# Kernel tuning notes

Hardware: AMD Instinct MI355X
Metric: run time of the kernel (lower is better)

The kernel has to match this reference:

```python
import jax, jax.numpy as jnp
import numpy as np

N, E, IN, H, OUT, G = 50000, 600000, 128, 128, 10, 64


def gcn_conv(x, src, dst, W, b, n):
    # PyG GCNConv: x' = D^{-1/2} (A + I) D^{-1/2} (x W) + b
    h = x @ W
    ones = jnp.ones(src.shape[0], x.dtype)
    deg = jax.ops.segment_sum(ones, dst, num_segments=n) + 1.0  # +1 for self-loop
    dinv = jax.lax.rsqrt(deg)
    norm = dinv[src] * dinv[dst]                                 # [E]
    agg = jax.ops.segment_sum(h[src] * norm[:, None], dst, num_segments=n)
    agg = agg + h * (1.0 / deg)[:, None]                         # self-loop term
    return agg + b


def setup_inputs() -> dict:
    key = jax.random.key(0)
    ks = jax.random.split(key, 12)
    s = 1.0 / np.sqrt(H)
    return {
        "x": jax.random.normal(ks[0], (N, IN), jnp.float32),
        "edge_index": jax.random.randint(ks[1], (2, E), 0, N, dtype=jnp.int32),
        "batch": jnp.sort(jax.random.randint(ks[2], (N,), 0, G, dtype=jnp.int32)),
        "W1": jax.random.normal(ks[3], (IN, H), jnp.float32) * s,
        "b1": jnp.zeros((H,), jnp.float32),
        "W2": jax.random.normal(ks[4], (H, H), jnp.float32) * s,
        "b2": jnp.zeros((H,), jnp.float32),
        "W3": jax.random.normal(ks[5], (H, H), jnp.float32) * s,
        "b3": jnp.zeros((H,), jnp.float32),
        "Wfc": jax.random.normal(ks[6], (H, OUT), jnp.float32) * s,
        "bfc": jnp.zeros((OUT,), jnp.float32),
    }


def reference(x, edge_index, batch, W1, b1, W2, b2, W3, b3, Wfc, bfc):
    src, dst = edge_index[0], edge_index[1]
    h = jax.nn.relu(gcn_conv(x, src, dst, W1, b1, N))
    h = jax.nn.relu(gcn_conv(h, src, dst, W2, b2, N))
    h = jax.nn.relu(gcn_conv(h, src, dst, W3, b3, N))
    # global mean pool over graphs
    sums = jax.ops.segment_sum(h, batch, num_segments=G)
    cnt = jax.ops.segment_sum(jnp.ones(N, h.dtype), batch, num_segments=G)
    pooled = sums / jnp.maximum(cnt, 1.0)[:, None]               # [G, H]
    return pooled @ Wfc + bfc                                    # [G, OUT]
```

## Files before the change

### kernel.cpp

```cpp
#include <hip/hip_runtime.h>


#define N_NODES 50000
#define N_EDGES 600000
#define DIM 128
#define OUT_DIM 10
#define N_GRAPHS 64
#define STRIP 128
#define GR 64

__global__ void zero_kernel(int* __restrict__ p, int n) {
    int i = blockIdx.x * blockDim.x + threadIdx.x;
    for (; i < n; i += gridDim.x * blockDim.x) p[i] = 0;
}

__global__ void hist_kernel(const int* __restrict__ dst, int* __restrict__ deg) {
    int e = blockIdx.x * blockDim.x + threadIdx.x;
    if (e < N_EDGES) atomicAdd(&deg[dst[e]], 1);
}

__global__ void node_prep_kernel(const int* __restrict__ deg, int* __restrict__ start,
                                 float* __restrict__ dinv, float* __restrict__ invdeg,
                                 int* __restrict__ gcur) {
    int i = blockIdx.x * blockDim.x + threadIdx.x;
    if (i < N_NODES) {
        int d = deg[i];
        start[i] = atomicAdd(gcur, d);
        float df = (float)d + 1.0f;
        dinv[i]   = rsqrtf(df);
        invdeg[i] = 1.0f / df;
    }
}

__global__ void csr_build_kernel(const int* __restrict__ src, const int* __restrict__ dst,
                                 const int* __restrict__ start, int* __restrict__ cursor,
                                 const float* __restrict__ dinv,
                                 int2* __restrict__ csr_pair) {
    int e = blockIdx.x * blockDim.x + threadIdx.x;
    if (e < N_EDGES) {
        int s = src[e], d = dst[e];
        int slot = start[d] + atomicAdd(&cursor[d], 1);
        int2 rec;
        rec.x = s;
        rec.y = __float_as_int(dinv[s] * dinv[d]);
        csr_pair[slot] = rec;
    }
}

__global__ __launch_bounds__(256) void gemm_kernel(const float* __restrict__ A,
                                                   const float* __restrict__ W,
                                                   float* __restrict__ C) {
    __shared__ float4 Alds[GR][DIM / 4];
    int row0 = blockIdx.x * GR;
    int tid  = threadIdx.x;
    for (int i = tid; i < GR * (DIM / 4); i += 256) {
        int r = i >> 5, c = i & 31;
        int gr = row0 + r;
        Alds[r][c] = (gr < N_NODES) ? ((const float4*)A)[(size_t)gr * 32 + c]
                                    : make_float4(0.f, 0.f, 0.f, 0.f);
    }
    __syncthreads();
    int tx = tid & 31;
    int ty = tid >> 5;
    float acc[8][4];
#pragma unroll
    for (int r = 0; r < 8; ++r)
#pragma unroll
        for (int c = 0; c < 4; ++c) acc[r][c] = 0.f;
    const float4* W4 = (const float4*)W;
    for (int k = 0; k < DIM; k += 4) {
        float4 a[8];
#pragma unroll
        for (int r = 0; r < 8; ++r) a[r] = Alds[ty * 8 + r][k >> 2];
        float4 w0 = W4[(k + 0) * 32 + tx];
        float4 w1 = W4[(k + 1) * 32 + tx];
        float4 w2 = W4[(k + 2) * 32 + tx];
        float4 w3 = W4[(k + 3) * 32 + tx];
#pragma unroll
        for (int r = 0; r < 8; ++r) {
            acc[r][0] += a[r].x * w0.x + a[r].y * w1.x + a[r].z * w2.x + a[r].w * w3.x;
            acc[r][1] += a[r].x * w0.y + a[r].y * w1.y + a[r].z * w2.y + a[r].w * w3.y;
            acc[r][2] += a[r].x * w0.z + a[r].y * w1.z + a[r].z * w2.z + a[r].w * w3.z;
            acc[r][3] += a[r].x * w0.w + a[r].y * w1.w + a[r].z * w2.w + a[r].w * w3.w;
        }
    }
#pragma unroll
    for (int r = 0; r < 8; ++r) {
        int gr = row0 + ty * 8 + r;
        if (gr < N_NODES) {
            float4 o = make_float4(acc[r][0], acc[r][1], acc[r][2], acc[r][3]);
            ((float4*)C)[(size_t)gr * 32 + tx] = o;
        }
    }
}

__global__ __launch_bounds__(256) void pull_kernel(const float* __restrict__ HW,
                                                   const int2* __restrict__ csr_pair,
                                                   const int* __restrict__ start,
                                                   const int* __restrict__ deg,
                                                   const float* __restrict__ invdeg,
                                                   const float* __restrict__ bias,
                                                   float* __restrict__ Fout) {
    int node = blockIdx.x * 4 + (threadIdx.x >> 6);
    int lane = threadIdx.x & 63;
    if (node >= N_NODES) return;
    const float2* HW2 = (const float2*)HW;
    int st = start[node];
    int dg = deg[node];
    float ax = 0.f, ay = 0.f;
    for (int base = 0; base < dg; base += 64) {
        int m = min(dg - base, 64);
        int2 rec = (lane < m) ? csr_pair[st + base + lane] : make_int2(0, 0);
        int   si = rec.x;
        float wi = __int_as_float(rec.y);
        int idx = 0;
        for (; idx + 8 <= m; idx += 8) {
            int s0 = __shfl(si, idx);     int s1 = __shfl(si, idx + 1);
            int s2 = __shfl(si, idx + 2); int s3 = __shfl(si, idx + 3);
            int s4 = __shfl(si, idx + 4); int s5 = __shfl(si, idx + 5);
            int s6 = __shfl(si, idx + 6); int s7 = __shfl(si, idx + 7);
            float w0 = __shfl(wi, idx);     float w1 = __shfl(wi, idx + 1);
            float w2 = __shfl(wi, idx + 2); float w3 = __shfl(wi, idx + 3);
            float w4 = __shfl(wi, idx + 4); float w5 = __shfl(wi, idx + 5);
            float w6 = __shfl(wi, idx + 6); float w7 = __shfl(wi, idx + 7);
            float2 v0 = HW2[(size_t)s0 * 64 + lane];
            float2 v1 = HW2[(size_t)s1 * 64 + lane];
            float2 v2 = HW2[(size_t)s2 * 64 + lane];
            float2 v3 = HW2[(size_t)s3 * 64 + lane];
            float2 v4 = HW2[(size_t)s4 * 64 + lane];
            float2 v5 = HW2[(size_t)s5 * 64 + lane];
            float2 v6 = HW2[(size_t)s6 * 64 + lane];
            float2 v7 = HW2[(size_t)s7 * 64 + lane];
            ax += v0.x * w0; ay += v0.y * w0;
            ax += v1.x * w1; ay += v1.y * w1;
            ax += v2.x * w2; ay += v2.y * w2;
            ax += v3.x * w3; ay += v3.y * w3;
            ax += v4.x * w4; ay += v4.y * w4;
            ax += v5.x * w5; ay += v5.y * w5;
            ax += v6.x * w6; ay += v6.y * w6;
            ax += v7.x * w7; ay += v7.y * w7;
        }
        for (; idx < m; ++idx) {
            int s = __shfl(si, idx);
            float w = __shfl(wi, idx);
            float2 v = HW2[(size_t)s * 64 + lane];
            ax += v.x * w; ay += v.y * w;
        }
    }
    float iv = invdeg[node];
    float2 hs = HW2[(size_t)node * 64 + lane];
    ax += hs.x * iv; ay += hs.y * iv;
    float2 bb = ((const float2*)bias)[lane];
    ax = fmaxf(ax + bb.x, 0.f);
    ay = fmaxf(ay + bb.y, 0.f);
    float2 o; o.x = ax; o.y = ay;
    ((float2*)Fout)[(size_t)node * 64 + lane] = o;
}

__global__ void bounds_kernel(const int* __restrict__ batch,
                              int* __restrict__ startg, int* __restrict__ endg) {
    int i = blockIdx.x * blockDim.x + threadIdx.x;
    if (i >= N_NODES) return;
    int b = batch[i];
    if (i == 0 || batch[i - 1] != b) startg[b] = i;
    if (i == N_NODES - 1 || batch[i + 1] != b) endg[b] = i + 1;
}

__global__ __launch_bounds__(128) void pool_kernel(const float* __restrict__ F,
                                                   const int* __restrict__ batch,
                                                   float* __restrict__ pooled) {
    int s0 = blockIdx.x * STRIP;
    int f  = threadIdx.x;
    if (s0 >= N_NODES) return;
    int end = min(s0 + STRIP, N_NODES);
    int cur = batch[s0];
    float acc = 0.f;
    for (int n = s0; n < end; ++n) {
        int bn = batch[n];
        if (bn != cur) {
            atomicAdd(&pooled[cur * DIM + f], acc);
            acc = 0.f; cur = bn;
        }
        acc += F[(size_t)n * DIM + f];
    }
    atomicAdd(&pooled[cur * DIM + f], acc);
}

__global__ __launch_bounds__(640) void fc_kernel(const float* __restrict__ pooled,
                                                 const int* __restrict__ startg,
                                                 const int* __restrict__ endg,
                                                 const float* __restrict__ Wfc,
                                                 const float* __restrict__ bfc,
                                                 float* __restrict__ out) {
    int t = threadIdx.x;
    if (t >= N_GRAPHS * OUT_DIM) return;
    int g = t / OUT_DIM, o = t % OUT_DIM;
    int c = endg[g] - startg[g];
    float inv = 1.0f / fmaxf((float)c, 1.0f);
    float acc = bfc[o];
#pragma unroll 8
    for (int k = 0; k < DIM; ++k)
        acc += pooled[g * DIM + k] * inv * Wfc[k * OUT_DIM + o];
    out[g * OUT_DIM + o] = acc;
}

extern "C" void kernel_launch(void* const* d_in, const int* in_sizes, int n_in,
                              void* d_out, int out_size, void* d_ws, size_t ws_size,
                              hipStream_t stream) {
    const float* x    = (const float*)d_in[0];
    const int*   ei   = (const int*)d_in[1];
    const int*   batch= (const int*)d_in[2];
    const float* W1   = (const float*)d_in[3];
    const float* b1   = (const float*)d_in[4];
    const float* W2   = (const float*)d_in[5];
    const float* b2   = (const float*)d_in[6];
    const float* W3   = (const float*)d_in[7];
    const float* b3   = (const float*)d_in[8];
    const float* Wfc  = (const float*)d_in[9];
    const float* bfc  = (const float*)d_in[10];
    float* out = (float*)d_out;

    const int* src = ei;
    const int* dst = ei + N_EDGES;

    char* ws = (char*)d_ws;
    size_t o = 0;
    float* HW   = (float*)(ws + o); o += (size_t)N_NODES * DIM * 4;
    float* PB   = (float*)(ws + o); o += (size_t)N_NODES * DIM * 4;
    int*   deg    = (int*)(ws + o); o += (size_t)N_NODES * 4;
    int*   cursor = (int*)(ws + o); o += (size_t)N_NODES * 4;
    float* pooled = (float*)(ws + o); o += (size_t)N_GRAPHS * DIM * 4;
    int*   startg = (int*)(ws + o); o += (size_t)N_GRAPHS * 4;
    int*   endg   = (int*)(ws + o); o += (size_t)N_GRAPHS * 4;
    int*   gcur   = (int*)(ws + o); o += 4;
    o = (o + 7) & ~(size_t)7;
    int*   startv = (int*)(ws + o); o += (size_t)N_NODES * 4;
    float* dinv   = (float*)(ws + o); o += (size_t)N_NODES * 4;
    float* invdeg = (float*)(ws + o); o += (size_t)N_NODES * 4;
    int2*  csr_pair = (int2*)(ws + o); o += (size_t)N_EDGES * 8;

    const int nzero = 2 * N_NODES + N_GRAPHS * DIM + 2 * N_GRAPHS + 1;

    zero_kernel<<<(nzero + 255) / 256, 256, 0, stream>>>(deg, nzero);
    hist_kernel<<<(N_EDGES + 255) / 256, 256, 0, stream>>>(dst, deg);
    node_prep_kernel<<<(N_NODES + 255) / 256, 256, 0, stream>>>(deg, startv, dinv, invdeg, gcur);
    csr_build_kernel<<<(N_EDGES + 255) / 256, 256, 0, stream>>>(src, dst, startv, cursor,
                                                                dinv, csr_pair);

    const int ggrid = (N_NODES + GR - 1) / GR;
    const int pgrid = (N_NODES + 3) / 4;

    gemm_kernel<<<ggrid, 256, 0, stream>>>(x, W1, HW);
    pull_kernel<<<pgrid, 256, 0, stream>>>(HW, csr_pair, startv, deg, invdeg, b1, PB);
    gemm_kernel<<<ggrid, 256, 0, stream>>>(PB, W2, HW);
    pull_kernel<<<pgrid, 256, 0, stream>>>(HW, csr_pair, startv, deg, invdeg, b2, PB);
    gemm_kernel<<<ggrid, 256, 0, stream>>>(PB, W3, HW);
    pull_kernel<<<pgrid, 256, 0, stream>>>(HW, csr_pair, startv, deg, invdeg, b3, PB);

    bounds_kernel<<<(N_NODES + 255) / 256, 256, 0, stream>>>(batch, startg, endg);
    pool_kernel<<<(N_NODES + STRIP - 1) / STRIP, 128, 0, stream>>>(PB, batch, pooled);
    fc_kernel<<<1, 640, 0, stream>>>(pooled, startg, endg, Wfc, bfc, out);
}
```

Baseline: 441.7 us.

## Replace atomic CSR offsets with prefix scan and split pull across feature halves

Node start offsets were handed out by an atomic counter in arbitrary order. They are now computed by a three-kernel exclusive prefix scan, so each node's edge list sits in node order and consecutive nodes' edges are contiguous. The pull kernel now launches two blocks per group of four nodes, each covering 64 of the 128 features with scalar loads instead of float2. This doubles parallelism and shortens each wave's work, at the cost of re-reading the CSR records and shuffles twice and narrower memory transactions.

```diff
diff --git a/kernel.cpp b/kernel.cpp
--- a/kernel.cpp
+++ b/kernel.cpp
@@ -8,6 +8,7 @@
 #define N_GRAPHS 64
 #define STRIP 128
 #define GR 64
+#define SCAN_G ((N_NODES + 255) / 256)
 
 __global__ void zero_kernel(int* __restrict__ p, int n) {
     int i = blockIdx.x * blockDim.x + threadIdx.x;
@@ -19,17 +20,58 @@
     if (e < N_EDGES) atomicAdd(&deg[dst[e]], 1);
 }
 
-__global__ void node_prep_kernel(const int* __restrict__ deg, int* __restrict__ start,
-                                 float* __restrict__ dinv, float* __restrict__ invdeg,
-                                 int* __restrict__ gcur) {
-    int i = blockIdx.x * blockDim.x + threadIdx.x;
+__global__ __launch_bounds__(256) void scan_local_kernel(const int* __restrict__ deg,
+                                                         int* __restrict__ locx,
+                                                         int* __restrict__ bsum,
+                                                         float* __restrict__ dinv,
+                                                         float* __restrict__ invdeg) {
+    __shared__ int lds[256];
+    int tid = threadIdx.x;
+    int i = blockIdx.x * 256 + tid;
+    int d = (i < N_NODES) ? deg[i] : 0;
+    int v = d;
+    lds[tid] = v;
+    __syncthreads();
+#pragma unroll
+    for (int off = 1; off < 256; off <<= 1) {
+        int t = (tid >= off) ? lds[tid - off] : 0;
+        __syncthreads();
+        v += t;
+        lds[tid] = v;
+        __syncthreads();
+    }
     if (i < N_NODES) {
-        int d = deg[i];
-        start[i] = atomicAdd(gcur, d);
+        locx[i] = v - d;
         float df = (float)d + 1.0f;
         dinv[i]   = rsqrtf(df);
         invdeg[i] = 1.0f / df;
     }
+    if (tid == 255) bsum[blockIdx.x] = v;
+}
+
+__global__ __launch_bounds__(256) void scan_block_kernel(const int* __restrict__ bsum,
+                                                         int* __restrict__ boff) {
+    __shared__ int lds[256];
+    int tid = threadIdx.x;
+    int d = (tid < SCAN_G) ? bsum[tid] : 0;
+    int v = d;
+    lds[tid] = v;
+    __syncthreads();
+#pragma unroll
+    for (int off = 1; off < 256; off <<= 1) {
+        int t = (tid >= off) ? lds[tid - off] : 0;
+        __syncthreads();
+        v += t;
+        lds[tid] = v;
+        __syncthreads();
+    }
+    if (tid < SCAN_G) boff[tid] = v - d;
+}
+
+__global__ void scan_apply_kernel(const int* __restrict__ locx, const int* __restrict__ boff,
+                                  int* __restrict__ startv) {
+    int i = blockIdx.x * blockDim.x + threadIdx.x;
+    if (i < N_NODES) startv[i] = locx[i] + boff[blockIdx.x];
 }
 
 __global__ void csr_build_kernel(const int* __restrict__ src, const int* __restrict__ dst,
@@ -101,13 +143,15 @@
                                                    const float* __restrict__ invdeg,
                                                    const float* __restrict__ bias,
                                                    float* __restrict__ Fout) {
-    int node = blockIdx.x * 4 + (threadIdx.x >> 6);
+    int wid  = threadIdx.x >> 6;
     int lane = threadIdx.x & 63;
+    int half = blockIdx.x & 1;
+    int node = (blockIdx.x >> 1) * 4 + wid;
     if (node >= N_NODES) return;
-    const float2* HW2 = (const float2*)HW;
+    int f = half * 64 + lane;
     int st = start[node];
     int dg = deg[node];
-    float ax = 0.f, ay = 0.f;
+    float ax = 0.f;
     for (int base = 0; base < dg; base += 64) {
         int m = min(dg - base, 64);
         int2 rec = (lane < m) ? csr_pair[st + base + lane] : make_int2(0, 0);
@@ -123,38 +167,26 @@
             float w2 = __shfl(wi, idx + 2); float w3 = __shfl(wi, idx + 3);
             float w4 = __shfl(wi, idx + 4); float w5 = __shfl(wi, idx + 5);
             float w6 = __shfl(wi, idx + 6); float w7 = __shfl(wi, idx + 7);
-            float2 v0 = HW2[(size_t)s0 * 64 + lane];
-            float2 v1 = HW2[(size_t)s1 * 64 + lane];
-            float2 v2 = HW2[(size_t)s2 * 64 + lane];
-            float2 v3 = HW2[(size_t)s3 * 64 + lane];
-            float2 v4 = HW2[(size_t)s4 * 64 + lane];
-            float2 v5 = HW2[(size_t)s5 * 64 + lane];
-            float2 v6 = HW2[(size_t)s6 * 64 + lane];
-            float2 v7 = HW2[(size_t)s7 * 64 + lane];
-            ax += v0.x * w0; ay += v0.y * w0;
-            ax += v1.x * w1; ay += v1.y * w1;
-            ax += v2.x * w2; ay += v2.y * w2;
-            ax += v3.x * w3; ay += v3.y * w3;
-            ax += v4.x * w4; ay += v4.y * w4;
-            ax += v5.x * w5; ay += v5.y * w5;
-            ax += v6.x * w6; ay += v6.y * w6;
-            ax += v7.x * w7; ay += v7.y * w7;
+            float v0 = HW[(size_t)s0 * DIM + f];
+            float v1 = HW[(size_t)s1 * DIM + f];
+            float v2 = HW[(size_t)s2 * DIM + f];
+            float v3 = HW[(size_t)s3 * DIM + f];
+            float v4 = HW[(size_t)s4 * DIM + f];
+            float v5 = HW[(size_t)s5 * DIM + f];
+            float v6 = HW[(size_t)s6 * DIM + f];
+            float v7 = HW[(size_t)s7 * DIM + f];
+            ax += v0 * w0 + v1 * w1 + v2 * w2 + v3 * w3
+                + v4 * w4 + v5 * w5 + v6 * w6 + v7 * w7;
         }
         for (; idx < m; ++idx) {
             int s = __shfl(si, idx);
             float w = __shfl(wi, idx);
-            float2 v = HW2[(size_t)s * 64 + lane];
-            ax += v.x * w; ay += v.y * w;
-        }
-    }
-    float iv = invdeg[node];
-    float2 hs = HW2[(size_t)node * 64 + lane];
-    ax += hs.x * iv; ay += hs.y * iv;
-    float2 bb = ((const float2*)bias)[lane];
-    ax = fmaxf(ax + bb.x, 0.f);
-    ay = fmaxf(ay + bb.y, 0.f);
-    float2 o; o.x = ax; o.y = ay;
-    ((float2*)Fout)[(size_t)node * 64 + lane] = o;
+            ax += HW[(size_t)s * DIM + f] * w;
+        }
+    }
+    ax += HW[(size_t)node * DIM + f] * invdeg[node];
+    ax = fmaxf(ax + bias[f], 0.f);
+    Fout[(size_t)node * DIM + f] = ax;
 }
 
 __global__ void bounds_kernel(const int* __restrict__ batch,
@@ -232,23 +264,27 @@
     float* pooled = (float*)(ws + o); o += (size_t)N_GRAPHS * DIM * 4;
     int*   startg = (int*)(ws + o); o += (size_t)N_GRAPHS * 4;
     int*   endg   = (int*)(ws + o); o += (size_t)N_GRAPHS * 4;
-    int*   gcur   = (int*)(ws + o); o += 4;
-    o = (o + 7) & ~(size_t)7;
     int*   startv = (int*)(ws + o); o += (size_t)N_NODES * 4;
     float* dinv   = (float*)(ws + o); o += (size_t)N_NODES * 4;
     float* invdeg = (float*)(ws + o); o += (size_t)N_NODES * 4;
+    int*   locx   = (int*)(ws + o); o += (size_t)N_NODES * 4;
+    int*   bsum   = (int*)(ws + o); o += (size_t)SCAN_G * 4;
+    int*   boff   = (int*)(ws + o); o += (size_t)SCAN_G * 4;
+    o = (o + 7) & ~(size_t)7;
     int2*  csr_pair = (int2*)(ws + o); o += (size_t)N_EDGES * 8;
 
-    const int nzero = 2 * N_NODES + N_GRAPHS * DIM + 2 * N_GRAPHS + 1;
+    const int nzero = 2 * N_NODES + N_GRAPHS * DIM + 2 * N_GRAPHS;
 
     zero_kernel<<<(nzero + 255) / 256, 256, 0, stream>>>(deg, nzero);
     hist_kernel<<<(N_EDGES + 255) / 256, 256, 0, stream>>>(dst, deg);
-    node_prep_kernel<<<(N_NODES + 255) / 256, 256, 0, stream>>>(deg, startv, dinv, invdeg, gcur);
+    scan_local_kernel<<<SCAN_G, 256, 0, stream>>>(deg, locx, bsum, dinv, invdeg);
+    scan_block_kernel<<<1, 256, 0, stream>>>(bsum, boff);
+    scan_apply_kernel<<<SCAN_G, 256, 0, stream>>>(locx, boff, startv);
     csr_build_kernel<<<(N_EDGES + 255) / 256, 256, 0, stream>>>(src, dst, startv, cursor,
                                                                 dinv, csr_pair);
 
     const int ggrid = (N_NODES + GR - 1) / GR;
-    const int pgrid = (N_NODES + 3) / 4;
+    const int pgrid = 2 * ((N_NODES + 3) / 4);
 
     gemm_kernel<<<ggrid, 256, 0, stream>>>(x, W1, HW);
     pull_kernel<<<pgrid, 256, 0, stream>>>(HW, csr_pair, startv, deg, invdeg, b1, PB);
```

New measurement: 468.0 us. 5.9% more time.
